# Performance work log

Measured on AMD Instinct MI355X. Metric: run time of the kernel, lower is better.

The kernel has to match this reference:

```python
import jax, jax.numpy as jnp
import numpy as np

N_NODES = 50000
N_EDGES = 400000
N_GRAPHS = 500
N_FEAT = 4
EMB = 200
HID = 128


def setup_inputs() -> dict:
    key = jax.random.key(0)
    ks = jax.random.split(key, 16)
    x = jax.random.normal(ks[0], (N_NODES, N_FEAT), dtype=jnp.float32)
    edge_index = jax.random.randint(ks[1], (2, N_EDGES), 0, N_NODES, dtype=jnp.int64)
    x_scalar = jax.random.normal(ks[2], (N_GRAPHS, N_FEAT), dtype=jnp.float32)
    batch_index = jnp.sort(jax.random.randint(ks[3], (N_NODES,), 0, N_GRAPHS, dtype=jnp.int64))

    def lin(k, fan_in, fan_out):
        return jax.random.normal(k, (fan_in, fan_out), dtype=jnp.float32) / np.sqrt(fan_in)

    params = {
        'W0': lin(ks[4], N_FEAT, EMB), 'b0': jnp.zeros((EMB,), jnp.float32),
        'W1': lin(ks[5], EMB, EMB), 'b1': jnp.zeros((EMB,), jnp.float32),
        'W2': lin(ks[6], EMB, EMB), 'b2': jnp.zeros((EMB,), jnp.float32),
        'W3': lin(ks[7], EMB, EMB), 'b3': jnp.zeros((EMB,), jnp.float32),
        'Wl1': lin(ks[8], EMB + N_FEAT, HID),
        'bl1': jax.random.normal(ks[9], (HID,), jnp.float32) * 0.01,
        'Wl2': lin(ks[10], HID, 1),
        'bl2': jax.random.normal(ks[11], (1,), jnp.float32) * 0.01,
    }
    return dict(x=x, edge_index=edge_index, x_scalar=x_scalar, batch_index=batch_index, **params)


def _gcn_conv(h, W, b, src, dst, norm, num_nodes):
    # PyG GCNConv: h' = D^-1/2 (A+I) D^-1/2 (h W) + b, with precomputed edge norms
    m = (h @ W)[src] * norm[:, None]            # [E+N, out]
    out = jax.ops.segment_sum(m, dst, num_segments=num_nodes)
    return out + b


def reference(x, edge_index, x_scalar, batch_index,
              W0, b0, W1, b1, W2, b2, W3, b3, Wl1, bl1, Wl2, bl2):
    num_nodes = x.shape[0]
    loops = jnp.arange(num_nodes, dtype=edge_index.dtype)
    src = jnp.concatenate([edge_index[0], loops])  # self-loops appended
    dst = jnp.concatenate([edge_index[1], loops])
    deg = jax.ops.segment_sum(jnp.ones_like(dst, dtype=x.dtype), dst, num_segments=num_nodes)
    dinv = deg ** -0.5                              # deg >= 1 due to self-loops
    norm = dinv[src] * dinv[dst]

    h = jax.nn.leaky_relu(_gcn_conv(x, W0, b0, src, dst, norm, num_nodes), 0.01)
    h = jax.nn.leaky_relu(_gcn_conv(h, W1, b1, src, dst, norm, num_nodes), 0.01)
    h = jax.nn.leaky_relu(_gcn_conv(h, W2, b2, src, dst, norm, num_nodes), 0.01)
    h = jax.nn.leaky_relu(_gcn_conv(h, W3, b3, src, dst, norm, num_nodes), 0.01)

    # global mean pool per graph
    sums = jax.ops.segment_sum(h, batch_index, num_segments=N_GRAPHS)
    cnt = jax.ops.segment_sum(jnp.ones((num_nodes,), h.dtype), batch_index, num_segments=N_GRAPHS)
    pooled = sums / jnp.maximum(cnt, 1.0)[:, None]

    g = jnp.concatenate([pooled, x_scalar], axis=1)   # [G, EMB+4]
    g = jax.nn.leaky_relu(g @ Wl1 + bl1, 0.01)
    out = g @ Wl2 + bl2                                # [G, 1]
    return out
```

## Files before the change

### kernel.cpp

```cpp
#include <hip/hip_runtime.h>
#include <math.h>

#define LEAKY(v) ((v) > 0.0f ? (v) : 0.01f * (v))

typedef _Float16 v8h __attribute__((ext_vector_type(8)));
typedef float v4f __attribute__((ext_vector_type(4)));

__global__ void k_zero(int* __restrict__ cnt, int n) {
    int i = blockIdx.x * blockDim.x + threadIdx.x;
    if (i < n) cnt[i] = 0;
}

__global__ void k_count(const int* __restrict__ ei, int* __restrict__ cnt, int E) {
    int e = blockIdx.x * blockDim.x + threadIdx.x;
    if (e < E) atomicAdd(&cnt[ei[E + e]], 1);
}

__global__ __launch_bounds__(256) void k_scan1(const int* __restrict__ cnt,
                                               int* __restrict__ rowptr,
                                               int* __restrict__ bsum, int n) {
    __shared__ int s[256];
    int t = threadIdx.x, i = blockIdx.x * 256 + t;
    int v = (i < n) ? cnt[i] : 0;
    s[t] = v;
    __syncthreads();
    for (int off = 1; off < 256; off <<= 1) {
        int u = (t >= off) ? s[t - off] : 0;
        __syncthreads();
        s[t] += u;
        __syncthreads();
    }
    if (i < n) rowptr[i] = s[t] - v;
    if (t == 255) bsum[blockIdx.x] = s[255];
}

__global__ __launch_bounds__(256) void k_scan2(int* __restrict__ bsum, int nb) {
    __shared__ int s[256];
    int t = threadIdx.x;
    int v = (t < nb) ? bsum[t] : 0;
    s[t] = v;
    __syncthreads();
    for (int off = 1; off < 256; off <<= 1) {
        int u = (t >= off) ? s[t - off] : 0;
        __syncthreads();
        s[t] += u;
        __syncthreads();
    }
    if (t < nb) bsum[t] = s[t] - v;
}

__global__ __launch_bounds__(256) void k_scan3(int* __restrict__ rowptr,
                                               const int* __restrict__ bsum,
                                               const int* __restrict__ cnt,
                                               float* __restrict__ dinv, int n) {
    int i = blockIdx.x * 256 + threadIdx.x;
    if (i < n) {
        rowptr[i] += bsum[blockIdx.x];
        dinv[i] = rsqrtf(1.0f + (float)cnt[i]);
    }
}

__global__ void k_fill(const int* __restrict__ ei, const float* __restrict__ dinv,
                       int* __restrict__ rowptr, int2* __restrict__ adj, int E) {
    int e = blockIdx.x * blockDim.x + threadIdx.x;
    if (e < E) {
        int s = ei[e], d = ei[E + e];
        int pos = atomicAdd(&rowptr[d], 1);
        adj[pos] = make_int2(s, __float_as_int(dinv[s] * dinv[d]));
    }
}

__global__ __launch_bounds__(256) void k_splitW3(const float* __restrict__ W1,
                                                 const float* __restrict__ W2,
                                                 const float* __restrict__ W3,
                                                 _Float16* __restrict__ th0, _Float16* __restrict__ tl0,
                                                 _Float16* __restrict__ th1, _Float16* __restrict__ tl1,
                                                 _Float16* __restrict__ th2, _Float16* __restrict__ tl2) {
    int layer = blockIdx.y;
    const float* W = (layer == 0) ? W1 : (layer == 1) ? W2 : W3;
    _Float16* Wth = (layer == 0) ? th0 : (layer == 1) ? th1 : th2;
    _Float16* Wtl = (layer == 0) ? tl0 : (layer == 1) ? tl1 : tl2;
    int idx = blockIdx.x * blockDim.x + threadIdx.x;
    if (idx >= 224 * 208) return;
    int k = idx / 208, n = idx - k * 208;
    float v = (k < 200 && n < 200) ? W[k * 200 + n] : 0.0f;
    _Float16 hi = (_Float16)v;
    _Float16 lo = (_Float16)(v - (float)hi);
    Wth[n * 224 + k] = hi;
    Wtl[n * 224 + k] = lo;
}

__global__ void k_gather4(const float* __restrict__ x, const float* __restrict__ dinv,
                          const int* __restrict__ rowptr, const int2* __restrict__ adj,
                          float* __restrict__ px, int n) {
    int v = blockIdx.x * blockDim.x + threadIdx.x;
    if (v >= n) return;
    float w0 = dinv[v]; w0 *= w0;
    float4 xv = ((const float4*)x)[v];
    float4 acc = make_float4(xv.x * w0, xv.y * w0, xv.z * w0, xv.w * w0);
    int lo = v ? rowptr[v - 1] : 0;
    int hi = rowptr[v];
    for (int j = lo; j < hi; ++j) {
        int2 cw = adj[j];
        int s = cw.x; float w = __int_as_float(cw.y);
        float4 sv = ((const float4*)x)[s];
        acc.x += sv.x * w; acc.y += sv.y * w; acc.z += sv.z * w; acc.w += sv.w * w;
    }
    ((float4*)px)[v] = acc;
}

__global__ __launch_bounds__(256, 4) void k_gemm200_mfma_l0(const float* __restrict__ px,
                                                            const float* __restrict__ W0,
                                                            const float* __restrict__ b0,
                                                            const _Float16* __restrict__ Wth,
                                                            const _Float16* __restrict__ Wtl,
                                                            _Float16* __restrict__ T, int M) {
    __shared__ _Float16 Wsh[208 * 32];
    __shared__ _Float16 Wsl[208 * 32];
    __shared__ float W0s[4][200];
    __shared__ float b0s[200];
    const int tid  = threadIdx.x;
    const int lane = tid & 63;
    const int wid  = tid >> 6;
    const int quad = lane >> 4;
    const int l16  = lane & 15;
    const int rowA = blockIdx.x * 64 + wid * 16 + l16;
    const int rowAc = min(rowA, M - 1);
    const float4 pxv = ((const float4*)px)[rowAc];

    for (int idx = tid; idx < 1000; idx += 256) {
        if (idx < 800) W0s[idx / 200][idx % 200] = W0[idx];
        else b0s[idx - 800] = b0[idx - 800];
    }
    __syncthreads();

    v4f acc[13];
#pragma unroll
    for (int t = 0; t < 13; ++t) acc[t] = 0.0f;

    for (int k0 = 0; k0 < 224; k0 += 32) {
        v8h ah, al;
        int kb = k0 + quad * 8;
        if (kb < 200) {
#pragma unroll
            for (int j = 0; j < 8; ++j) {
                int k = kb + j;
                float pv = pxv.x * W0s[0][k] + pxv.y * W0s[1][k]
                         + pxv.z * W0s[2][k] + pxv.w * W0s[3][k] + b0s[k];
                pv = LEAKY(pv);
                _Float16 h = (_Float16)pv;
                ah[j] = h;
                al[j] = (_Float16)(pv - (float)h);
            }
        } else {
#pragma unroll
            for (int j = 0; j < 8; ++j) { ah[j] = (_Float16)0.0f; al[j] = (_Float16)0.0f; }
        }
        __syncthreads();
        for (int idx = tid; idx < 832; idx += 256) {
            int nr = idx >> 2, part = idx & 3;
            *(uint4*)&Wsh[nr * 32 + part * 8] = *(const uint4*)&Wth[nr * 224 + k0 + part * 8];
            *(uint4*)&Wsl[nr * 32 + part * 8] = *(const uint4*)&Wtl[nr * 224 + k0 + part * 8];
        }
        __syncthreads();
#pragma unroll
        for (int t = 0; t < 13; ++t) {
            int nidx = (t * 16 + l16) * 32 + quad * 8;
            v8h wh = *(const v8h*)&Wsh[nidx];
            v8h wl = *(const v8h*)&Wsl[nidx];
            acc[t] = __builtin_amdgcn_mfma_f32_16x16x32_f16(ah, wh, acc[t], 0, 0, 0);
            acc[t] = __builtin_amdgcn_mfma_f32_16x16x32_f16(ah, wl, acc[t], 0, 0, 0);
            acc[t] = __builtin_amdgcn_mfma_f32_16x16x32_f16(al, wh, acc[t], 0, 0, 0);
        }
    }
    const int rb = blockIdx.x * 64 + wid * 16 + quad * 4;
#pragma unroll
    for (int t = 0; t < 13; ++t) {
        int c = t * 16 + l16;
        if (c < 200) {
#pragma unroll
            for (int e = 0; e < 4; ++e) {
                int r = rb + e;
                if (r < M) T[(size_t)r * 200 + c] = (_Float16)acc[t][e];
            }
        }
    }
}

__global__ __launch_bounds__(256, 4) void k_gemm200_mfma(const float* __restrict__ P,
                                                         const float* __restrict__ bias,
                                                         const _Float16* __restrict__ Wth,
                                                         const _Float16* __restrict__ Wtl,
                                                         _Float16* __restrict__ T, int M) {
    __shared__ _Float16 Wsh[208 * 32];
    __shared__ _Float16 Wsl[208 * 32];
    const int tid  = threadIdx.x;
    const int lane = tid & 63;
    const int wid  = tid >> 6;
    const int quad = lane >> 4;
    const int l16  = lane & 15;
    const int rowA = blockIdx.x * 64 + wid * 16 + l16;
    const int rowAc = min(rowA, M - 1);
    const float* Prow = P + (size_t)rowAc * 200;

    v4f acc[13];
#pragma unroll
    for (int t = 0; t < 13; ++t) acc[t] = 0.0f;

    for (int k0 = 0; k0 < 224; k0 += 32) {
        v8h ah, al;
        int kb = k0 + quad * 8;
        if (kb < 200) {
            float4 pa = *(const float4*)(Prow + kb);
            float4 pb = *(const float4*)(Prow + kb + 4);
            float4 ba = *(const float4*)(bias + kb);
            float4 bb = *(const float4*)(bias + kb + 4);
            float av[8];
            av[0] = LEAKY(pa.x + ba.x); av[1] = LEAKY(pa.y + ba.y);
            av[2] = LEAKY(pa.z + ba.z); av[3] = LEAKY(pa.w + ba.w);
            av[4] = LEAKY(pb.x + bb.x); av[5] = LEAKY(pb.y + bb.y);
            av[6] = LEAKY(pb.z + bb.z); av[7] = LEAKY(pb.w + bb.w);
#pragma unroll
            for (int j = 0; j < 8; ++j) {
                _Float16 h = (_Float16)av[j];
                ah[j] = h;
                al[j] = (_Float16)(av[j] - (float)h);
            }
        } else {
#pragma unroll
            for (int j = 0; j < 8; ++j) { ah[j] = (_Float16)0.0f; al[j] = (_Float16)0.0f; }
        }
        __syncthreads();
        for (int idx = tid; idx < 832; idx += 256) {
            int nr = idx >> 2, part = idx & 3;
            *(uint4*)&Wsh[nr * 32 + part * 8] = *(const uint4*)&Wth[nr * 224 + k0 + part * 8];
            *(uint4*)&Wsl[nr * 32 + part * 8] = *(const uint4*)&Wtl[nr * 224 + k0 + part * 8];
        }
        __syncthreads();
#pragma unroll
        for (int t = 0; t < 13; ++t) {
            int nidx = (t * 16 + l16) * 32 + quad * 8;
            v8h wh = *(const v8h*)&Wsh[nidx];
            v8h wl = *(const v8h*)&Wsl[nidx];
            acc[t] = __builtin_amdgcn_mfma_f32_16x16x32_f16(ah, wh, acc[t], 0, 0, 0);
            acc[t] = __builtin_amdgcn_mfma_f32_16x16x32_f16(ah, wl, acc[t], 0, 0, 0);
            acc[t] = __builtin_amdgcn_mfma_f32_16x16x32_f16(al, wh, acc[t], 0, 0, 0);
        }
    }
    const int rb = blockIdx.x * 64 + wid * 16 + quad * 4;
#pragma unroll
    for (int t = 0; t < 13; ++t) {
        int c = t * 16 + l16;
        if (c < 200) {
#pragma unroll
            for (int e = 0; e < 4; ++e) {
                int r = rb + e;
                if (r < M) T[(size_t)r * 200 + c] = (_Float16)acc[t][e];
            }
        }
    }
}

__global__ __launch_bounds__(256) void k_gather200h(const _Float16* __restrict__ t,
                                                    const float* __restrict__ dinv,
                                                    const int* __restrict__ rowptr,
                                                    const int2* __restrict__ adj,
                                                    float* __restrict__ p, int n) {
    int gid = blockIdx.x * blockDim.x + threadIdx.x;
    if (gid >= n * 25) return;
    int v = gid / 25, c8 = gid - v * 25;
    const v8h* tp = (const v8h*)t;
    float w0 = dinv[v]; w0 *= w0;
    v8h tv = tp[v * 25 + c8];
    float a0[8], a1[8];
#pragma unroll
    for (int i = 0; i < 8; ++i) { a0[i] = (float)tv[i] * w0; a1[i] = 0.0f; }
    int lo = v ? rowptr[v - 1] : 0;
    int hi = rowptr[v];
    int j = lo;
    for (; j + 1 < hi; j += 2) {
        int2 e0 = adj[j], e1 = adj[j + 1];
        float wa = __int_as_float(e0.y), wb = __int_as_float(e1.y);
        v8h s0 = tp[e0.x * 25 + c8];
        v8h s1 = tp[e1.x * 25 + c8];
#pragma unroll
        for (int i = 0; i < 8; ++i) {
            a0[i] += (float)s0[i] * wa;
            a1[i] += (float)s1[i] * wb;
        }
    }
    if (j < hi) {
        int2 cw = adj[j];
        float w = __int_as_float(cw.y);
        v8h sv = tp[cw.x * 25 + c8];
#pragma unroll
        for (int i = 0; i < 8; ++i) a0[i] += (float)sv[i] * w;
    }
    float4 o0 = make_float4(a0[0] + a1[0], a0[1] + a1[1], a0[2] + a1[2], a0[3] + a1[3]);
    float4 o1 = make_float4(a0[4] + a1[4], a0[5] + a1[5], a0[6] + a1[6], a0[7] + a1[7]);
    ((float4*)p)[v * 50 + c8 * 2] = o0;
    ((float4*)p)[v * 50 + c8 * 2 + 1] = o1;
}

__global__ __launch_bounds__(256) void k_poolmlp(const float* __restrict__ p3,
                                                 const float* __restrict__ b3,
                                                 const int* __restrict__ batch, int n_nodes,
                                                 const float* __restrict__ xs,
                                                 const float* __restrict__ Wl1,
                                                 const float* __restrict__ bl1,
                                                 const float* __restrict__ Wl2,
                                                 const float* __restrict__ bl2,
                                                 float* __restrict__ out) {
    __shared__ float grow[204];
    __shared__ float partial[2];
    __shared__ int sb[2];
    int g = blockIdx.x;
    int t = threadIdx.x;
    if (t == 0) {
        int lo = 0, hi = n_nodes;
        while (lo < hi) { int m = (lo + hi) >> 1; if (batch[m] < g) lo = m + 1; else hi = m; }
        sb[0] = lo;
        int lo2 = lo, hi2 = n_nodes;
        while (lo2 < hi2) { int m = (lo2 + hi2) >> 1; if (batch[m] < g + 1) lo2 = m + 1; else hi2 = m; }
        sb[1] = lo2;
    }
    __syncthreads();
    int lo = sb[0], hi = sb[1];
    if (t < 200) {
        float bc = b3[t];
        float s = 0.0f;
        for (int i = lo; i < hi; ++i) {
            float v = p3[(size_t)i * 200 + t] + bc;
            s += LEAKY(v);
        }
        grow[t] = s / fmaxf((float)(hi - lo), 1.0f);
    }
    if (t < 4) grow[200 + t] = xs[g * 4 + t];
    __syncthreads();
    float hv = 0.0f;
    if (t < 128) {
        float s = bl1[t];
        for (int k = 0; k < 204; ++k) s += grow[k] * Wl1[k * 128 + t];
        s = LEAKY(s);
        hv = s * Wl2[t];
    }
    for (int off = 32; off > 0; off >>= 1) hv += __shfl_down(hv, off, 64);
    if (t < 128 && (t & 63) == 0) partial[t >> 6] = hv;
    __syncthreads();
    if (t == 0) out[g] = partial[0] + partial[1] + bl2[0];
}

extern "C" void kernel_launch(void* const* d_in, const int* in_sizes, int n_in,
                              void* d_out, int out_size, void* d_ws, size_t ws_size,
                              hipStream_t stream) {
    const float* x    = (const float*)d_in[0];
    const int*   ei   = (const int*)d_in[1];
    const float* xs   = (const float*)d_in[2];
    const int*   batch= (const int*)d_in[3];
    const float* W0   = (const float*)d_in[4];
    const float* b0   = (const float*)d_in[5];
    const float* W1   = (const float*)d_in[6];
    const float* b1   = (const float*)d_in[7];
    const float* W2   = (const float*)d_in[8];
    const float* b2   = (const float*)d_in[9];
    const float* W3   = (const float*)d_in[10];
    const float* b3   = (const float*)d_in[11];
    const float* Wl1  = (const float*)d_in[12];
    const float* bl1  = (const float*)d_in[13];
    const float* Wl2  = (const float*)d_in[14];
    const float* bl2  = (const float*)d_in[15];
    float* out = (float*)d_out;

    const int N = in_sizes[0] / 4;
    const int E = in_sizes[1] / 2;
    const int G = in_sizes[2] / 4;

    char* ws = (char*)d_ws;
    size_t off = 0;
    auto alloc = [&](size_t bytes) { void* p = ws + off; off += (bytes + 255) & ~size_t(255); return p; };
    float*    buf0 = (float*)alloc((size_t)N * 200 * sizeof(float));
    _Float16* bufh = (_Float16*)alloc((size_t)N * 200 * sizeof(_Float16));
    float* dinv   = (float*)alloc((size_t)N * sizeof(float));
    float* px     = (float*)alloc((size_t)N * 4 * sizeof(float));
    int*   cnt    = (int*)alloc((size_t)N * sizeof(int));
    int*   rowptr = (int*)alloc(((size_t)N + 1) * sizeof(int));
    int*   bsum   = (int*)alloc(256 * sizeof(int));
    int2*  adj    = (int2*)alloc((size_t)E * sizeof(int2));
    _Float16* Wth[3]; _Float16* Wtl[3];
    for (int i = 0; i < 3; ++i) {
        Wth[i] = (_Float16*)alloc(208 * 224 * sizeof(_Float16));
        Wtl[i] = (_Float16*)alloc(208 * 224 * sizeof(_Float16));
    }

    const int B = 256;
    const int nblk = (N + 255) / 256;
    k_zero<<<(N + B - 1) / B, B, 0, stream>>>(cnt, N);
    k_count<<<(E + B - 1) / B, B, 0, stream>>>(ei, cnt, E);
    k_scan1<<<nblk, 256, 0, stream>>>(cnt, rowptr, bsum, N);
    k_scan2<<<1, 256, 0, stream>>>(bsum, nblk);
    k_scan3<<<nblk, 256, 0, stream>>>(rowptr, bsum, cnt, dinv, N);
    k_fill<<<(E + B - 1) / B, B, 0, stream>>>(ei, dinv, rowptr, adj, E);

    dim3 sg((224 * 208 + B - 1) / B, 3);
    k_splitW3<<<sg, B, 0, stream>>>(W1, W2, W3, Wth[0], Wtl[0], Wth[1], Wtl[1], Wth[2], Wtl[2]);

    k_gather4<<<(N + B - 1) / B, B, 0, stream>>>(x, dinv, rowptr, adj, px, N);

    const int gblocks = (N * 25 + 255) / 256;

    k_gemm200_mfma_l0<<<(N + 63) / 64, 256, 0, stream>>>(px, W0, b0, Wth[0], Wtl[0], bufh, N);
    k_gather200h<<<gblocks, 256, 0, stream>>>(bufh, dinv, rowptr, adj, buf0, N);

    k_gemm200_mfma<<<(N + 63) / 64, 256, 0, stream>>>(buf0, b1, Wth[1], Wtl[1], bufh, N);
    k_gather200h<<<gblocks, 256, 0, stream>>>(bufh, dinv, rowptr, adj, buf0, N);
    k_gemm200_mfma<<<(N + 63) / 64, 256, 0, stream>>>(buf0, b2, Wth[2], Wtl[2], bufh, N);
    k_gather200h<<<gblocks, 256, 0, stream>>>(bufh, dinv, rowptr, adj, buf0, N);

    k_poolmlp<<<G, 256, 0, stream>>>(buf0, b3, batch, N, xs, Wl1, bl1, Wl2, bl2, out);
}
```

Baseline: 390.9 us.

## Store aggregated activations in fp16 and parallelize mean pooling across node chunks

The gather kernel now writes its aggregated output as fp16 instead of fp32, and the next GEMM reads fp16 directly. This halves the write traffic of each gather and the read traffic of each GEMM. Pooling is split into a chunked kernel that does segmented sums with atomics into a zeroed per-graph buffer, plus a small MLP kernel, replacing the old one-block-per-graph serial loop. The risk is reduced precision in the intermediate activations, plus atomic contention at graph boundaries.

```diff
diff --git a/kernel.cpp b/kernel.cpp
--- a/kernel.cpp
+++ b/kernel.cpp
@@ -9,6 +9,11 @@
 __global__ void k_zero(int* __restrict__ cnt, int n) {
     int i = blockIdx.x * blockDim.x + threadIdx.x;
     if (i < n) cnt[i] = 0;
+}
+
+__global__ void k_zerof(float* __restrict__ p, int n) {
+    int i = blockIdx.x * blockDim.x + threadIdx.x;
+    if (i < n) p[i] = 0.0f;
 }
 
 __global__ void k_count(const int* __restrict__ ei, int* __restrict__ cnt, int E) {
@@ -187,7 +192,7 @@
     }
 }
 
-__global__ __launch_bounds__(256, 4) void k_gemm200_mfma(const float* __restrict__ P,
+__global__ __launch_bounds__(256, 4) void k_gemm200_mfma(const _Float16* __restrict__ P,
                                                          const float* __restrict__ bias,
                                                          const _Float16* __restrict__ Wth,
                                                          const _Float16* __restrict__ Wtl,
@@ -201,7 +206,7 @@
     const int l16  = lane & 15;
     const int rowA = blockIdx.x * 64 + wid * 16 + l16;
     const int rowAc = min(rowA, M - 1);
-    const float* Prow = P + (size_t)rowAc * 200;
+    const _Float16* Prow = P + (size_t)rowAc * 200;
 
     v4f acc[13];
 #pragma unroll
@@ -211,20 +216,17 @@
         v8h ah, al;
         int kb = k0 + quad * 8;
         if (kb < 200) {
-            float4 pa = *(const float4*)(Prow + kb);
-            float4 pb = *(const float4*)(Prow + kb + 4);
+            v8h ph = *(const v8h*)(Prow + kb);
             float4 ba = *(const float4*)(bias + kb);
             float4 bb = *(const float4*)(bias + kb + 4);
-            float av[8];
-            av[0] = LEAKY(pa.x + ba.x); av[1] = LEAKY(pa.y + ba.y);
-            av[2] = LEAKY(pa.z + ba.z); av[3] = LEAKY(pa.w + ba.w);
-            av[4] = LEAKY(pb.x + bb.x); av[5] = LEAKY(pb.y + bb.y);
-            av[6] = LEAKY(pb.z + bb.z); av[7] = LEAKY(pb.w + bb.w);
+            float bv[8] = {ba.x, ba.y, ba.z, ba.w, bb.x, bb.y, bb.z, bb.w};
 #pragma unroll
             for (int j = 0; j < 8; ++j) {
-                _Float16 h = (_Float16)av[j];
+                float av = (float)ph[j] + bv[j];
+                av = LEAKY(av);
+                _Float16 h = (_Float16)av;
                 ah[j] = h;
-                al[j] = (_Float16)(av[j] - (float)h);
+                al[j] = (_Float16)(av - (float)h);
             }
         } else {
 #pragma unroll
@@ -265,7 +267,7 @@
                                                     const float* __restrict__ dinv,
                                                     const int* __restrict__ rowptr,
                                                     const int2* __restrict__ adj,
-                                                    float* __restrict__ p, int n) {
+                                                    _Float16* __restrict__ p, int n) {
     int gid = blockIdx.x * blockDim.x + threadIdx.x;
     if (gid >= n * 25) return;
     int v = gid / 25, c8 = gid - v * 25;
@@ -296,21 +298,45 @@
 #pragma unroll
         for (int i = 0; i < 8; ++i) a0[i] += (float)sv[i] * w;
     }
-    float4 o0 = make_float4(a0[0] + a1[0], a0[1] + a1[1], a0[2] + a1[2], a0[3] + a1[3]);
-    float4 o1 = make_float4(a0[4] + a1[4], a0[5] + a1[5], a0[6] + a1[6], a0[7] + a1[7]);
-    ((float4*)p)[v * 50 + c8 * 2] = o0;
-    ((float4*)p)[v * 50 + c8 * 2 + 1] = o1;
-}
-
-__global__ __launch_bounds__(256) void k_poolmlp(const float* __restrict__ p3,
+    v8h o;
+#pragma unroll
+    for (int i = 0; i < 8; ++i) o[i] = (_Float16)(a0[i] + a1[i]);
+    ((v8h*)p)[v * 25 + c8] = o;
+}
+
+__global__ __launch_bounds__(256) void k_poolsum(const _Float16* __restrict__ p3,
                                                  const float* __restrict__ b3,
-                                                 const int* __restrict__ batch, int n_nodes,
-                                                 const float* __restrict__ xs,
-                                                 const float* __restrict__ Wl1,
-                                                 const float* __restrict__ bl1,
-                                                 const float* __restrict__ Wl2,
-                                                 const float* __restrict__ bl2,
-                                                 float* __restrict__ out) {
+                                                 const int* __restrict__ batch, int n,
+                                                 float* __restrict__ pooled) {
+    int c = threadIdx.x;
+    if (c >= 200) return;
+    int base = blockIdx.x * 64;
+    int end = min(base + 64, n);
+    float bc = b3[c];
+    int gprev = batch[base];
+    float s = 0.0f;
+    for (int i = base; i < end; ++i) {
+        int g = batch[i];
+        float v = (float)p3[(size_t)i * 200 + c] + bc;
+        v = LEAKY(v);
+        if (g != gprev) {
+            atomicAdd(&pooled[gprev * 200 + c], s);
+            s = 0.0f;
+            gprev = g;
+        }
+        s += v;
+    }
+    atomicAdd(&pooled[gprev * 200 + c], s);
+}
+
+__global__ __launch_bounds__(128) void k_mlpfin(const float* __restrict__ pooled,
+                                                const int* __restrict__ batch, int n_nodes,
+                                                const float* __restrict__ xs,
+                                                const float* __restrict__ Wl1,
+                                                const float* __restrict__ bl1,
+                                                const float* __restrict__ Wl2,
+                                                const float* __restrict__ bl2,
+                                                float* __restrict__ out) {
     __shared__ float grow[204];
     __shared__ float partial[2];
     __shared__ int sb[2];
@@ -325,27 +351,16 @@
         sb[1] = lo2;
     }
     __syncthreads();
-    int lo = sb[0], hi = sb[1];
-    if (t < 200) {
-        float bc = b3[t];
-        float s = 0.0f;
-        for (int i = lo; i < hi; ++i) {
-            float v = p3[(size_t)i * 200 + t] + bc;
-            s += LEAKY(v);
-        }
-        grow[t] = s / fmaxf((float)(hi - lo), 1.0f);
-    }
+    float inv = 1.0f / fmaxf((float)(sb[1] - sb[0]), 1.0f);
+    for (int idx = t; idx < 200; idx += 128) grow[idx] = pooled[g * 200 + idx] * inv;
     if (t < 4) grow[200 + t] = xs[g * 4 + t];
     __syncthreads();
-    float hv = 0.0f;
-    if (t < 128) {
-        float s = bl1[t];
-        for (int k = 0; k < 204; ++k) s += grow[k] * Wl1[k * 128 + t];
-        s = LEAKY(s);
-        hv = s * Wl2[t];
-    }
+    float s = bl1[t];
+    for (int k = 0; k < 204; ++k) s += grow[k] * Wl1[k * 128 + t];
+    s = LEAKY(s);
+    float hv = s * Wl2[t];
     for (int off = 32; off > 0; off >>= 1) hv += __shfl_down(hv, off, 64);
-    if (t < 128 && (t & 63) == 0) partial[t >> 6] = hv;
+    if ((t & 63) == 0) partial[t >> 6] = hv;
     __syncthreads();
     if (t == 0) out[g] = partial[0] + partial[1] + bl2[0];
 }
@@ -378,10 +393,11 @@
     char* ws = (char*)d_ws;
     size_t off = 0;
     auto alloc = [&](size_t bytes) { void* p = ws + off; off += (bytes + 255) & ~size_t(255); return p; };
-    float*    buf0 = (float*)alloc((size_t)N * 200 * sizeof(float));
-    _Float16* bufh = (_Float16*)alloc((size_t)N * 200 * sizeof(_Float16));
+    _Float16* bufA = (_Float16*)alloc((size_t)N * 200 * sizeof(_Float16));
+    _Float16* bufB = (_Float16*)alloc((size_t)N * 200 * sizeof(_Float16));
     float* dinv   = (float*)alloc((size_t)N * sizeof(float));
     float* px     = (float*)alloc((size_t)N * 4 * sizeof(float));
+    float* pooled = (float*)alloc((size_t)G * 200 * sizeof(float));
     int*   cnt    = (int*)alloc((size_t)N * sizeof(int));
     int*   rowptr = (int*)alloc(((size_t)N + 1) * sizeof(int));
     int*   bsum   = (int*)alloc(256 * sizeof(int));
@@ -401,6 +417,8 @@
     k_scan3<<<nblk, 256, 0, stream>>>(rowptr, bsum, cnt, dinv, N);
     k_fill<<<(E + B - 1) / B, B, 0, stream>>>(ei, dinv, rowptr, adj, E);
 
+    k_zerof<<<(G * 200 + B - 1) / B, B, 0, stream>>>(pooled, G * 200);
+
     dim3 sg((224 * 208 + B - 1) / B, 3);
     k_splitW3<<<sg, B, 0, stream>>>(W1, W2, W3, Wth[0], Wtl[0], Wth[1], Wtl[1], Wth[2], Wtl[2]);
 
@@ -408,13 +426,14 @@
 
     const int gblocks = (N * 25 + 255) / 256;
 
-    k_gemm200_mfma_l0<<<(N + 63) / 64, 256, 0, stream>>>(px, W0, b0, Wth[0], Wtl[0], bufh, N);
-    k_gather200h<<<gblocks, 256, 0, stream>>>(bufh, dinv, rowptr, adj, buf0, N);
-
-    k_gemm200_mfma<<<(N + 63) / 64, 256, 0, stream>>>(buf0, b1, Wth[1], Wtl[1], bufh, N);
-    k_gather200h<<<gblocks, 256, 0, stream>>>(bufh, dinv, rowptr, adj, buf0, N);
-    k_gemm200_mfma<<<(N + 63) / 64, 256, 0, stream>>>(buf0, b2, Wth[2], Wtl[2], bufh, N);
-    k_gather200h<<<gblocks, 256, 0, stream>>>(bufh, dinv, rowptr, adj, buf0, N);
-
-    k_poolmlp<<<G, 256, 0, stream>>>(buf0, b3, batch, N, xs, Wl1, bl1, Wl2, bl2, out);
-}
+    k_gemm200_mfma_l0<<<(N + 63) / 64, 256, 0, stream>>>(px, W0, b0, Wth[0], Wtl[0], bufA, N);
+    k_gather200h<<<gblocks, 256, 0, stream>>>(bufA, dinv, rowptr, adj, bufB, N);
+
+    k_gemm200_mfma<<<(N + 63) / 64, 256, 0, stream>>>(bufB, b1, Wth[1], Wtl[1], bufA, N);
+    k_gather200h<<<gblocks, 256, 0, stream>>>(bufA, dinv, rowptr, adj, bufB, N);
+    k_gemm200_mfma<<<(N + 63) / 64, 256, 0, stream>>>(bufB, b2, Wth[2], Wtl[2], bufA, N);
+    k_gather200h<<<gblocks, 256, 0, stream>>>(bufA, dinv, rowptr, adj, bufB, N);
+
+    k_poolsum<<<(N + 63) / 64, 256, 0, stream>>>(bufB, b3, batch, N, pooled);
+    k_mlpfin<<<G, 128, 0, stream>>>(pooled, batch, N, xs, Wl1, bl1, Wl2, bl2, out);
+}
```

Measured after the change: 365.3 us. 6.5% less time.
